# Kernel optimization log

Measured on AMD Instinct MI355X. Metric: run time of the kernel, lower is better.

Reference implementation:

```python
import jax, jax.numpy as jnp
import numpy as np


def setup_inputs() -> dict:
    key = jax.random.key(0)
    ks = jax.random.split(key, 8)
    B, CAST, H, IN = 2048, 128, 256, 256
    return {
        "x": jax.random.normal(ks[0], (B, IN), dtype=jnp.float32),
        "batch_idxs": jnp.arange(B, dtype=jnp.int64),
        "actor_ids": jax.random.randint(ks[1], (B,), 0, CAST).astype(jnp.int64),
        "story_stop_idxs": jax.random.randint(ks[2], (128,), 0, B).astype(jnp.int64),
        "state": jax.random.normal(ks[3], (B, CAST, H), dtype=jnp.float32),
        "w_ih": jax.random.normal(ks[4], (3 * H, IN), dtype=jnp.float32) * 0.05,
        "w_hh": jax.random.normal(ks[5], (3 * H, H), dtype=jnp.float32) * 0.05,
        "b_ih": jax.random.normal(ks[6], (3 * H,), dtype=jnp.float32) * 0.05,
        "b_hh": jax.random.normal(ks[7], (3 * H,), dtype=jnp.float32) * 0.05,
    }


def _gru_cell(x, h, w_ih, w_hh, b_ih, b_hh):
    # torch.nn.GRUCell math
    H = h.shape[-1]
    gi = x @ w_ih.T + b_ih  # [n, 3H]
    gh = h @ w_hh.T + b_hh  # [n, 3H]
    i_r, i_z, i_n = gi[:, :H], gi[:, H:2 * H], gi[:, 2 * H:]
    h_r, h_z, h_n = gh[:, :H], gh[:, H:2 * H], gh[:, 2 * H:]
    r = jax.nn.sigmoid(i_r + h_r)
    z = jax.nn.sigmoid(i_z + h_z)
    n = jnp.tanh(i_n + r * h_n)
    return (1.0 - z) * n + z * h


def reference(x, batch_idxs, actor_ids, story_stop_idxs, state, w_ih, w_hh, b_ih, b_hh):
    cast_size = state.shape[1]
    actor_ids = jnp.clip(actor_ids, 0, cast_size - 1)
    aid = actor_ids[batch_idxs]  # convert_idxs: actor slot per active story
    # gather indexed actor states
    selected = state[batch_idxs, aid]  # [n_active, H]
    # GRU-cell update
    new_selected = _gru_cell(x, selected, w_ih, w_hh, b_ih, b_hh)
    # scatter back into persistent memory
    new_state = state.at[batch_idxs, aid].set(new_selected)
    # zero out finished stories
    new_state = new_state.at[story_stop_idxs].set(0.0)
    return new_selected, new_state
```

## Files before the change

### kernel.cpp

```cpp
#include <hip/hip_runtime.h>

#define B_TOTAL 2048
#define CAST    128
#define HDIM    256
#define INDIM   256
#define BM      8
#define GRU_BLOCKS  (B_TOTAL / BM)
#define COPY_BLOCKS 2048

__global__ __launch_bounds__(256) void k_init(int* slot_aid, int* stop) {
    int t = blockIdx.x * blockDim.x + threadIdx.x;
    if (t < B_TOTAL) { slot_aid[t] = -1; stop[t] = 0; }
}

__global__ __launch_bounds__(256) void k_prep(
    const int* __restrict__ batch_idxs, const int* __restrict__ actor_ids,
    const int* __restrict__ story_stop, int n_stop,
    const float* __restrict__ w_ih, const float* __restrict__ w_hh,
    int* slot_aid, int* stop, float* wtI, float* wtH) {
    const int h = threadIdx.x;
    if (blockIdx.x < 8) {
        int t = blockIdx.x * 256 + h;
        int row = batch_idxs[t];
        int a = actor_ids[row];
        a = a < 0 ? 0 : (a > CAST - 1 ? CAST - 1 : a);
        slot_aid[row] = a;
        if (t < n_stop) stop[story_stop[t]] = 1;
    } else {
        int id  = blockIdx.x - 8;
        int mat = id / 192;
        int rem = id % 192;
        int g   = rem / 64;
        int k4  = rem % 64;
        const float* w = mat ? w_hh : w_ih;
        float*      wt = mat ? wtH  : wtI;
        float4 wv = *(const float4*)(w + ((size_t)(g * HDIM + h) * INDIM + k4 * 4));
        *(float4*)(wt + ((size_t)((k4 * 3 + g) * HDIM + h)) * 4) = wv;
    }
}

__global__ __launch_bounds__(256) void k_fused(
    const float* __restrict__ x, const int* __restrict__ batch_idxs,
    const int* __restrict__ actor_ids, const float* __restrict__ state,
    const float* __restrict__ wtI, const float* __restrict__ wtH,
    const float* __restrict__ b_ih, const float* __restrict__ b_hh,
    const int* __restrict__ slot_aid, const int* __restrict__ stop,
    float* __restrict__ out_sel, float* __restrict__ out_state) {
    __shared__ float xs[BM][INDIM];
    __shared__ float ss[BM][HDIM];
    const int h = threadIdx.x;

    if (blockIdx.x < GRU_BLOCKS) {
        const int b0 = blockIdx.x * BM;
        #pragma unroll
        for (int r = 0; r < BM; ++r) {
            int g  = b0 + r;
            int bi = batch_idxs[g];
            int a  = actor_ids[bi];
            a = a < 0 ? 0 : (a > CAST - 1 ? CAST - 1 : a);
            xs[r][h] = x[(size_t)g * INDIM + h];
            ss[r][h] = state[((size_t)bi * CAST + a) * HDIM + h];
        }
        __syncthreads();

        float air[BM], aiz[BM], ain[BM], ahr[BM], ahz[BM], ahn[BM];
        #pragma unroll
        for (int r = 0; r < BM; ++r) { air[r]=0.f; aiz[r]=0.f; ain[r]=0.f; ahr[r]=0.f; ahz[r]=0.f; ahn[r]=0.f; }

        const float4* __restrict__ wtI4 = (const float4*)wtI;
        const float4* __restrict__ wtH4 = (const float4*)wtH;

        for (int k4 = 0; k4 < INDIM / 4; ++k4) {
            float4 wir = wtI4[(k4 * 3 + 0) * HDIM + h];
            float4 wiz = wtI4[(k4 * 3 + 1) * HDIM + h];
            float4 win = wtI4[(k4 * 3 + 2) * HDIM + h];
            float4 whr = wtH4[(k4 * 3 + 0) * HDIM + h];
            float4 whz = wtH4[(k4 * 3 + 1) * HDIM + h];
            float4 whn = wtH4[(k4 * 3 + 2) * HDIM + h];
            #pragma unroll
            for (int r = 0; r < BM; ++r) {
                float4 xv = *(const float4*)(&xs[r][k4 * 4]);
                float4 sv = *(const float4*)(&ss[r][k4 * 4]);
                air[r] = fmaf(xv.w, wir.w, fmaf(xv.z, wir.z, fmaf(xv.y, wir.y, fmaf(xv.x, wir.x, air[r]))));
                aiz[r] = fmaf(xv.w, wiz.w, fmaf(xv.z, wiz.z, fmaf(xv.y, wiz.y, fmaf(xv.x, wiz.x, aiz[r]))));
                ain[r] = fmaf(xv.w, win.w, fmaf(xv.z, win.z, fmaf(xv.y, win.y, fmaf(xv.x, win.x, ain[r]))));
                ahr[r] = fmaf(sv.w, whr.w, fmaf(sv.z, whr.z, fmaf(sv.y, whr.y, fmaf(sv.x, whr.x, ahr[r]))));
                ahz[r] = fmaf(sv.w, whz.w, fmaf(sv.z, whz.z, fmaf(sv.y, whz.y, fmaf(sv.x, whz.x, ahz[r]))));
                ahn[r] = fmaf(sv.w, whn.w, fmaf(sv.z, whn.z, fmaf(sv.y, whn.y, fmaf(sv.x, whn.x, ahn[r]))));
            }
        }

        const float bir = b_ih[h], biz = b_ih[HDIM + h], bin = b_ih[2 * HDIM + h];
        const float bhr = b_hh[h], bhz = b_hh[HDIM + h], bhn = b_hh[2 * HDIM + h];

        #pragma unroll
        for (int r = 0; r < BM; ++r) {
            int g  = b0 + r;
            int bi = batch_idxs[g];
            int a  = actor_ids[bi];
            a = a < 0 ? 0 : (a > CAST - 1 ? CAST - 1 : a);
            float ir = air[r] + bir, iz = aiz[r] + biz, inn = ain[r] + bin;
            float hr = ahr[r] + bhr, hz = ahz[r] + bhz, hn = ahn[r] + bhn;
            float rr = 1.f / (1.f + __expf(-(ir + hr)));
            float zz = 1.f / (1.f + __expf(-(iz + hz)));
            float nn = tanhf(inn + rr * hn);
            float val = (1.f - zz) * nn + zz * ss[r][h];
            out_sel[(size_t)g * HDIM + h] = val;
            if (!stop[bi]) out_state[((size_t)bi * CAST + a) * HDIM + h] = val;
        }
    } else {
        const int  cb = blockIdx.x - GRU_BLOCKS;
        const long stride = (long)COPY_BLOCKS * 256;
        const long base = (long)cb * 256 + h;
        const float4* __restrict__ st4 = (const float4*)state;
        float4* __restrict__ out4 = (float4*)out_state;
        const float4 zero = make_float4(0.f, 0.f, 0.f, 0.f);
        #pragma unroll 2
        for (int it = 0; it < 32; it += 4) {
            long v0 = base + (long)(it + 0) * stride;
            long v1 = base + (long)(it + 1) * stride;
            long v2 = base + (long)(it + 2) * stride;
            long v3 = base + (long)(it + 3) * stride;
            float4 d0 = st4[v0], d1 = st4[v1], d2 = st4[v2], d3 = st4[v3];
            {
                int r = (int)(v0 >> 13), c = (int)((v0 >> 6) & (CAST - 1));
                if (stop[r]) out4[v0] = zero; else if (slot_aid[r] != c) out4[v0] = d0;
            }
            {
                int r = (int)(v1 >> 13), c = (int)((v1 >> 6) & (CAST - 1));
                if (stop[r]) out4[v1] = zero; else if (slot_aid[r] != c) out4[v1] = d1;
            }
            {
                int r = (int)(v2 >> 13), c = (int)((v2 >> 6) & (CAST - 1));
                if (stop[r]) out4[v2] = zero; else if (slot_aid[r] != c) out4[v2] = d2;
            }
            {
                int r = (int)(v3 >> 13), c = (int)((v3 >> 6) & (CAST - 1));
                if (stop[r]) out4[v3] = zero; else if (slot_aid[r] != c) out4[v3] = d3;
            }
        }
    }
}

extern "C" void kernel_launch(void* const* d_in, const int* in_sizes, int n_in,
                              void* d_out, int out_size, void* d_ws, size_t ws_size,
                              hipStream_t stream) {
    const float* x          = (const float*)d_in[0];
    const int*   batch_idxs = (const int*)d_in[1];
    const int*   actor_ids  = (const int*)d_in[2];
    const int*   story_stop = (const int*)d_in[3];
    const float* state      = (const float*)d_in[4];
    const float* w_ih       = (const float*)d_in[5];
    const float* w_hh       = (const float*)d_in[6];
    const float* b_ih       = (const float*)d_in[7];
    const float* b_hh       = (const float*)d_in[8];
    const int    n_stop     = in_sizes[3];

    float* out_sel   = (float*)d_out;
    float* out_state = out_sel + (size_t)B_TOTAL * HDIM;

    int*   slot_aid = (int*)d_ws;
    int*   stop     = slot_aid + B_TOTAL;
    float* wtI      = (float*)((char*)d_ws + 16384);
    float* wtH      = wtI + (size_t)3 * HDIM * INDIM;

    k_init<<<(B_TOTAL + 255) / 256, 256, 0, stream>>>(slot_aid, stop);
    k_prep<<<8 + 384, 256, 0, stream>>>(batch_idxs, actor_ids, story_stop, n_stop,
                                        w_ih, w_hh, slot_aid, stop, wtI, wtH);
    k_fused<<<GRU_BLOCKS + COPY_BLOCKS, 256, 0, stream>>>(
        x, batch_idxs, actor_ids, state, wtI, wtH, b_ih, b_hh,
        slot_aid, stop, out_sel, out_state);
}
```

Before: 170.5 us.

## Split fused kernel into GRU and per-row copy kernels with skipped reads for stopped rows

```diff
diff --git a/kernel.cpp b/kernel.cpp
--- a/kernel.cpp
+++ b/kernel.cpp
@@ -5,27 +5,27 @@
 #define HDIM    256
 #define INDIM   256
 #define BM      8
-#define GRU_BLOCKS  (B_TOTAL / BM)
-#define COPY_BLOCKS 2048
+#define GRU_BLOCKS (B_TOTAL / BM)
+#define ROW_F4     (CAST * HDIM / 4)
 
-__global__ __launch_bounds__(256) void k_init(int* slot_aid, int* stop) {
+__global__ __launch_bounds__(256) void k_init(int* rowaid, int* rowstop) {
     int t = blockIdx.x * blockDim.x + threadIdx.x;
-    if (t < B_TOTAL) { slot_aid[t] = -1; stop[t] = 0; }
+    if (t < B_TOTAL) { rowaid[t] = -1; rowstop[t] = 0; }
 }
 
 __global__ __launch_bounds__(256) void k_prep(
     const int* __restrict__ batch_idxs, const int* __restrict__ actor_ids,
     const int* __restrict__ story_stop, int n_stop,
     const float* __restrict__ w_ih, const float* __restrict__ w_hh,
-    int* slot_aid, int* stop, float* wtI, float* wtH) {
+    int* rowaid, int* rowstop, float* wtI, float* wtH) {
     const int h = threadIdx.x;
     if (blockIdx.x < 8) {
         int t = blockIdx.x * 256 + h;
         int row = batch_idxs[t];
         int a = actor_ids[row];
         a = a < 0 ? 0 : (a > CAST - 1 ? CAST - 1 : a);
-        slot_aid[row] = a;
-        if (t < n_stop) stop[story_stop[t]] = 1;
+        rowaid[row] = a;
+        if (t < n_stop) rowstop[story_stop[t]] = 1;
     } else {
         int id  = blockIdx.x - 8;
         int mat = id / 192;
@@ -39,105 +39,103 @@
     }
 }
 
-__global__ __launch_bounds__(256) void k_fused(
+__global__ __launch_bounds__(256) void k_gru(
     const float* __restrict__ x, const int* __restrict__ batch_idxs,
     const int* __restrict__ actor_ids, const float* __restrict__ state,
     const float* __restrict__ wtI, const float* __restrict__ wtH,
     const float* __restrict__ b_ih, const float* __restrict__ b_hh,
-    const int* __restrict__ slot_aid, const int* __restrict__ stop,
+    const int* __restrict__ rowstop,
     float* __restrict__ out_sel, float* __restrict__ out_state) {
     __shared__ float xs[BM][INDIM];
     __shared__ float ss[BM][HDIM];
-    const int h = threadIdx.x;
+    const int h  = threadIdx.x;
+    const int b0 = blockIdx.x * BM;
 
-    if (blockIdx.x < GRU_BLOCKS) {
-        const int b0 = blockIdx.x * BM;
+    #pragma unroll
+    for (int r = 0; r < BM; ++r) {
+        int g  = b0 + r;
+        int bi = batch_idxs[g];
+        int a  = actor_ids[bi];
+        a = a < 0 ? 0 : (a > CAST - 1 ? CAST - 1 : a);
+        xs[r][h] = x[(size_t)g * INDIM + h];
+        ss[r][h] = state[((size_t)bi * CAST + a) * HDIM + h];
+    }
+    __syncthreads();
+
+    float air[BM], aiz[BM], ain[BM], ahr[BM], ahz[BM], ahn[BM];
+    #pragma unroll
+    for (int r = 0; r < BM; ++r) { air[r]=0.f; aiz[r]=0.f; ain[r]=0.f; ahr[r]=0.f; ahz[r]=0.f; ahn[r]=0.f; }
+
+    const float4* __restrict__ wtI4 = (const float4*)wtI;
+    const float4* __restrict__ wtH4 = (const float4*)wtH;
+
+    for (int k4 = 0; k4 < INDIM / 4; ++k4) {
+        float4 wir = wtI4[(k4 * 3 + 0) * HDIM + h];
+        float4 wiz = wtI4[(k4 * 3 + 1) * HDIM + h];
+        float4 win = wtI4[(k4 * 3 + 2) * HDIM + h];
+        float4 whr = wtH4[(k4 * 3 + 0) * HDIM + h];
+        float4 whz = wtH4[(k4 * 3 + 1) * HDIM + h];
+        float4 whn = wtH4[(k4 * 3 + 2) * HDIM + h];
         #pragma unroll
         for (int r = 0; r < BM; ++r) {
-            int g  = b0 + r;
-            int bi = batch_idxs[g];
-            int a  = actor_ids[bi];
-            a = a < 0 ? 0 : (a > CAST - 1 ? CAST - 1 : a);
-            xs[r][h] = x[(size_t)g * INDIM + h];
-            ss[r][h] = state[((size_t)bi * CAST + a) * HDIM + h];
+            float4 xv = *(const float4*)(&xs[r][k4 * 4]);
+            float4 sv = *(const float4*)(&ss[r][k4 * 4]);
+            air[r] = fmaf(xv.w, wir.w, fmaf(xv.z, wir.z, fmaf(xv.y, wir.y, fmaf(xv.x, wir.x, air[r]))));
+            aiz[r] = fmaf(xv.w, wiz.w, fmaf(xv.z, wiz.z, fmaf(xv.y, wiz.y, fmaf(xv.x, wiz.x, aiz[r]))));
+            ain[r] = fmaf(xv.w, win.w, fmaf(xv.z, win.z, fmaf(xv.y, win.y, fmaf(xv.x, win.x, ain[r]))));
+            ahr[r] = fmaf(sv.w, whr.w, fmaf(sv.z, whr.z, fmaf(sv.y, whr.y, fmaf(sv.x, whr.x, ahr[r]))));
+            ahz[r] = fmaf(sv.w, whz.w, fmaf(sv.z, whz.z, fmaf(sv.y, whz.y, fmaf(sv.x, whz.x, ahz[r]))));
+            ahn[r] = fmaf(sv.w, whn.w, fmaf(sv.z, whn.z, fmaf(sv.y, whn.y, fmaf(sv.x, whn.x, ahn[r]))));
         }
-        __syncthreads();
+    }
 
-        float air[BM], aiz[BM], ain[BM], ahr[BM], ahz[BM], ahn[BM];
+    const float bir = b_ih[h], biz = b_ih[HDIM + h], bin = b_ih[2 * HDIM + h];
+    const float bhr = b_hh[h], bhz = b_hh[HDIM + h], bhn = b_hh[2 * HDIM + h];
+
+    #pragma unroll
+    for (int r = 0; r < BM; ++r) {
+        int g  = b0 + r;
+        int bi = batch_idxs[g];
+        int a  = actor_ids[bi];
+        a = a < 0 ? 0 : (a > CAST - 1 ? CAST - 1 : a);
+        float ir = air[r] + bir, iz = aiz[r] + biz, inn = ain[r] + bin;
+        float hr = ahr[r] + bhr, hz = ahz[r] + bhz, hn = ahn[r] + bhn;
+        float rr = 1.f / (1.f + __expf(-(ir + hr)));
+        float zz = 1.f / (1.f + __expf(-(iz + hz)));
+        float nn = tanhf(inn + rr * hn);
+        float val = (1.f - zz) * nn + zz * ss[r][h];
+        out_sel[(size_t)g * HDIM + h] = val;
+        if (!rowstop[bi]) out_state[((size_t)bi * CAST + a) * HDIM + h] = val;
+    }
+}
+
+__global__ __launch_bounds__(256) void k_copy(
+    const float4* __restrict__ st4, const int* __restrict__ rowaid,
+    const int* __restrict__ rowstop, float4* __restrict__ out4) {
+    const int  b = blockIdx.x;
+    const int  t = threadIdx.x;
+    const long base = (long)b * ROW_F4;
+    const int  aid = rowaid[b];
+
+    if (rowstop[b]) {
+        const float4 z = make_float4(0.f, 0.f, 0.f, 0.f);
         #pragma unroll
-        for (int r = 0; r < BM; ++r) { air[r]=0.f; aiz[r]=0.f; ain[r]=0.f; ahr[r]=0.f; ahz[r]=0.f; ahn[r]=0.f; }
+        for (int it = 0; it < ROW_F4 / 256; ++it)
+            out4[base + it * 256 + t] = z;
+        return;
+    }
 
-        const float4* __restrict__ wtI4 = (const float4*)wtI;
-        const float4* __restrict__ wtH4 = (const float4*)wtH;
-
-        for (int k4 = 0; k4 < INDIM / 4; ++k4) {
-            float4 wir = wtI4[(k4 * 3 + 0) * HDIM + h];
-            float4 wiz = wtI4[(k4 * 3 + 1) * HDIM + h];
-            float4 win = wtI4[(k4 * 3 + 2) * HDIM + h];
-            float4 whr = wtH4[(k4 * 3 + 0) * HDIM + h];
-            float4 whz = wtH4[(k4 * 3 + 1) * HDIM + h];
-            float4 whn = wtH4[(k4 * 3 + 2) * HDIM + h];
-            #pragma unroll
-            for (int r = 0; r < BM; ++r) {
-                float4 xv = *(const float4*)(&xs[r][k4 * 4]);
-                float4 sv = *(const float4*)(&ss[r][k4 * 4]);
-                air[r] = fmaf(xv.w, wir.w, fmaf(xv.z, wir.z, fmaf(xv.y, wir.y, fmaf(xv.x, wir.x, air[r]))));
-                aiz[r] = fmaf(xv.w, wiz.w, fmaf(xv.z, wiz.z, fmaf(xv.y, wiz.y, fmaf(xv.x, wiz.x, aiz[r]))));
-                ain[r] = fmaf(xv.w, win.w, fmaf(xv.z, win.z, fmaf(xv.y, win.y, fmaf(xv.x, win.x, ain[r]))));
-                ahr[r] = fmaf(sv.w, whr.w, fmaf(sv.z, whr.z, fmaf(sv.y, whr.y, fmaf(sv.x, whr.x, ahr[r]))));
-                ahz[r] = fmaf(sv.w, whz.w, fmaf(sv.z, whz.z, fmaf(sv.y, whz.y, fmaf(sv.x, whz.x, ahz[r]))));
-                ahn[r] = fmaf(sv.w, whn.w, fmaf(sv.z, whn.z, fmaf(sv.y, whn.y, fmaf(sv.x, whn.x, ahn[r]))));
-            }
-        }
-
-        const float bir = b_ih[h], biz = b_ih[HDIM + h], bin = b_ih[2 * HDIM + h];
-        const float bhr = b_hh[h], bhz = b_hh[HDIM + h], bhn = b_hh[2 * HDIM + h];
-
+    #pragma unroll
+    for (int g = 0; g < 4; ++g) {
+        float4 d[8];
         #pragma unroll
-        for (int r = 0; r < BM; ++r) {
-            int g  = b0 + r;
-            int bi = batch_idxs[g];
-            int a  = actor_ids[bi];
-            a = a < 0 ? 0 : (a > CAST - 1 ? CAST - 1 : a);
-            float ir = air[r] + bir, iz = aiz[r] + biz, inn = ain[r] + bin;
-            float hr = ahr[r] + bhr, hz = ahz[r] + bhz, hn = ahn[r] + bhn;
-            float rr = 1.f / (1.f + __expf(-(ir + hr)));
-            float zz = 1.f / (1.f + __expf(-(iz + hz)));
-            float nn = tanhf(inn + rr * hn);
-            float val = (1.f - zz) * nn + zz * ss[r][h];
-            out_sel[(size_t)g * HDIM + h] = val;
-            if (!stop[bi]) out_state[((size_t)bi * CAST + a) * HDIM + h] = val;
-        }
-    } else {
-        const int  cb = blockIdx.x - GRU_BLOCKS;
-        const long stride = (long)COPY_BLOCKS * 256;
-        const long base = (long)cb * 256 + h;
-        const float4* __restrict__ st4 = (const float4*)state;
-        float4* __restrict__ out4 = (float4*)out_state;
-        const float4 zero = make_float4(0.f, 0.f, 0.f, 0.f);
-        #pragma unroll 2
-        for (int it = 0; it < 32; it += 4) {
-            long v0 = base + (long)(it + 0) * stride;
-            long v1 = base + (long)(it + 1) * stride;
-            long v2 = base + (long)(it + 2) * stride;
-            long v3 = base + (long)(it + 3) * stride;
-            float4 d0 = st4[v0], d1 = st4[v1], d2 = st4[v2], d3 = st4[v3];
-            {
-                int r = (int)(v0 >> 13), c = (int)((v0 >> 6) & (CAST - 1));
-                if (stop[r]) out4[v0] = zero; else if (slot_aid[r] != c) out4[v0] = d0;
-            }
-            {
-                int r = (int)(v1 >> 13), c = (int)((v1 >> 6) & (CAST - 1));
-                if (stop[r]) out4[v1] = zero; else if (slot_aid[r] != c) out4[v1] = d1;
-            }
-            {
-                int r = (int)(v2 >> 13), c = (int)((v2 >> 6) & (CAST - 1));
-                if (stop[r]) out4[v2] = zero; else if (slot_aid[r] != c) out4[v2] = d2;
-            }
-            {
-                int r = (int)(v3 >> 13), c = (int)((v3 >> 6) & (CAST - 1));
-                if (stop[r]) out4[v3] = zero; else if (slot_aid[r] != c) out4[v3] = d3;
-            }
+        for (int i = 0; i < 8; ++i)
+            d[i] = st4[base + (g * 8 + i) * 256 + t];
+        #pragma unroll
+        for (int i = 0; i < 8; ++i) {
+            int idx = (g * 8 + i) * 256 + t;
+            if ((idx >> 6) != aid)
+                out4[base + idx] = d[i];
         }
     }
 }
@@ -159,15 +157,17 @@
     float* out_sel   = (float*)d_out;
     float* out_state = out_sel + (size_t)B_TOTAL * HDIM;
 
-    int*   slot_aid = (int*)d_ws;
-    int*   stop     = slot_aid + B_TOTAL;
-    float* wtI      = (float*)((char*)d_ws + 16384);
-    float* wtH      = wtI + (size_t)3 * HDIM * INDIM;
+    int*   rowaid  = (int*)d_ws;
+    int*   rowstop = rowaid + B_TOTAL;
+    float* wtI     = (float*)((char*)d_ws + 16384);
+    float* wtH     = wtI + (size_t)3 * HDIM * INDIM;
 
-    k_init<<<(B_TOTAL + 255) / 256, 256, 0, stream>>>(slot_aid, stop);
+    k_init<<<(B_TOTAL + 255) / 256, 256, 0, stream>>>(rowaid, rowstop);
     k_prep<<<8 + 384, 256, 0, stream>>>(batch_idxs, actor_ids, story_stop, n_stop,
-                                        w_ih, w_hh, slot_aid, stop, wtI, wtH);
-    k_fused<<<GRU_BLOCKS + COPY_BLOCKS, 256, 0, stream>>>(
-        x, batch_idxs, actor_ids, state, wtI, wtH, b_ih, b_hh,
-        slot_aid, stop, out_sel, out_state);
+                                        w_ih, w_hh, rowaid, rowstop, wtI, wtH);
+    k_gru<<<GRU_BLOCKS, 256, 0, stream>>>(x, batch_idxs, actor_ids, state,
+                                          wtI, wtH, b_ih, b_hh, rowstop,
+                                          out_sel, out_state);
+    k_copy<<<B_TOTAL, 256, 0, stream>>>((const float4*)state, rowaid, rowstop,
+                                        (float4*)out_state);
 }
```

Result: slower. 213.6 us (+25.3%).
